# Performance work log

Hardware: AMD Instinct MI355X
Metric: run time of the kernel (lower is better)

The kernel has to match this reference:

```python
import jax, jax.numpy as jnp
import numpy as np

N_HEADS = 16

def kernel_sigmoid(x):
    return jax.nn.sigmoid(0.6053 * x - 4.102)

def setup_inputs() -> dict:
    key = jax.random.key(0)
    kq, kk, kv = jax.random.split(key, 3)
    B, LQ, LK, E = 4, 4096, 4096, 1024
    return {
        "Q": jax.random.normal(kq, (B, LQ, E), dtype=jnp.float32),
        "K": jax.random.normal(kk, (B, LK, E), dtype=jnp.float32),
        "V": jax.random.normal(kv, (B, LK, E), dtype=jnp.float32),
    }

def reference(Q, K, V):
    B, LQ, E = Q.shape
    LK = K.shape[1]
    H = N_HEADS
    D = E // H
    # split heads -> [B, H, L, D]
    Qh = Q.reshape(B, LQ, H, D).transpose(0, 2, 1, 3)
    Kh = K.reshape(B, LK, H, D).transpose(0, 2, 1, 3)
    Vh = V.reshape(B, LK, H, D).transpose(0, 2, 1, 3)
    phi_Q = kernel_sigmoid(Qh)           # [B,H,LQ,D]
    phi_K = kernel_sigmoid(Kh)           # [B,H,LK,D]
    # KV state: phi_K^T @ V -> [B,H,D,D]
    kv = jnp.einsum("bhkd,bhke->bhde", phi_K, Vh)
    num = jnp.einsum("bhqd,bhde->bhqe", phi_Q, kv)      # [B,H,LQ,D]
    k_sum = phi_K.sum(axis=2)                            # [B,H,D]
    den = jnp.einsum("bhqd,bhd->bhq", phi_Q, k_sum)      # [B,H,LQ]
    out = num / den[..., None]
    # merge heads -> [B, LQ, E]
    return out.transpose(0, 2, 1, 3).reshape(B, LQ, E)
```

## Files before the change

kernel.cpp:

```cpp
#include <hip/hip_runtime.h>
#include <cstdint>
#include <cstddef>

#define B_ 4
#define L_ 4096
#define E_ 1024
#define H_ 16
#define D_ 64
#define BH_ 64
#define ST2_ 4160
#define NCH_ 16
#define RPC_ (L_/NCH_)
#define NT_ (RPC_/32)

typedef __attribute__((ext_vector_type(8))) short short8v;
typedef __attribute__((ext_vector_type(4))) float f32x4;

__device__ __forceinline__ float sigk(float x) {
    return __builtin_amdgcn_rcpf(1.0f + __expf(4.102f - 0.6053f * x));
}
__device__ __forceinline__ unsigned short bfh(float f) {
    union { float f; unsigned u; } v; v.f = f;
    const unsigned r = v.u + 0x7fffu + ((v.u >> 16) & 1u);
    return (unsigned short)(r >> 16);
}
__device__ __forceinline__ float bf2f(unsigned short s) {
    union { unsigned u; float f; } v; v.u = ((unsigned)s) << 16;
    return v.f;
}


__global__ void __launch_bounds__(256) kv_partial_kernel(
    const float* __restrict__ K, const float* __restrict__ V,
    float* __restrict__ partial)
{
    __shared__ short8v Bfrag[2 * 8 * 64];

    const int ch = blockIdx.x & (NCH_ - 1);
    const int bh = blockIdx.x / NCH_;
    const int b = bh >> 4, h = bh & 15;
    const int tid = threadIdx.x;
    const int w = tid >> 6, l = tid & 63;
    const int g = l >> 4, m = l & 15;
    const int k4 = g << 2;
    const int col = (w << 4) + m;

    const float* Kp = K + (size_t)(b * L_ + ch * RPC_) * E_ + h * D_ + col;
    const float* Vp = V + (size_t)(b * L_ + ch * RPC_) * E_ + h * D_ + col;

    f32x4 acc[4];
    #pragma unroll
    for (int t = 0; t < 4; ++t) acc[t] = (f32x4){0.f, 0.f, 0.f, 0.f};
    float ksacc = 0.f;

    float kr[2][8], vr[2][8];
    #pragma unroll
    for (int j = 0; j < 8; ++j) {
        const int ko = k4 + (j & 3) + ((j >> 2) << 4);
        kr[0][j] = Kp[(size_t)ko * E_];
        vr[0][j] = Vp[(size_t)ko * E_];
    }
    {
        short8v Bh, Bl;
        #pragma unroll
        for (int j = 0; j < 8; ++j) {
            const unsigned short hb = bfh(vr[0][j]);
            Bh[j] = (short)hb;
            Bl[j] = (short)bfh(vr[0][j] - bf2f(hb));
        }
        Bfrag[(w << 1) * 64 + l]       = Bh;
        Bfrag[((w << 1) + 1) * 64 + l] = Bl;
    }
    #pragma unroll
    for (int j = 0; j < 8; ++j) {
        const int ko = 32 + k4 + (j & 3) + ((j >> 2) << 4);
        kr[1][j] = Kp[(size_t)ko * E_];
        vr[1][j] = Vp[(size_t)ko * E_];
    }
    asm volatile("s_waitcnt lgkmcnt(0)" ::: "memory");
    __builtin_amdgcn_sched_barrier(0);
    __builtin_amdgcn_s_barrier();

    #pragma unroll 2
    for (int t = 0; t < NT_; ++t) {
        const int cur = t & 1, nxt = cur ^ 1;
        short8v Ah;
        #pragma unroll
        for (int j = 0; j < 8; ++j) {
            const unsigned short hb = bfh(sigk(kr[cur][j]));
            Ah[j] = (short)hb;
            ksacc += bf2f(hb);
        }
        if (t + 2 < NT_) {
            #pragma unroll
            for (int j = 0; j < 8; ++j) {
                const int ko = ((t + 2) << 5) + k4 + (j & 3) + ((j >> 2) << 4);
                kr[cur][j] = Kp[(size_t)ko * E_];
                vr[cur][j] = Vp[(size_t)ko * E_];
            }
        }
        __builtin_amdgcn_sched_barrier(0);
        {
            const int buf = cur << 9;
            #pragma unroll
            for (int tt = 0; tt < 4; ++tt) {
                const short8v Bh = Bfrag[buf + (tt << 1) * 64 + l];
                const short8v Bl = Bfrag[buf + ((tt << 1) + 1) * 64 + l];
                acc[tt] = __builtin_amdgcn_mfma_f32_16x16x32_bf16(Ah, Bh, acc[tt], 0, 0, 0);
                acc[tt] = __builtin_amdgcn_mfma_f32_16x16x32_bf16(Ah, Bl, acc[tt], 0, 0, 0);
            }
        }
        if (t + 1 < NT_) {
            const int nb = nxt << 9;
            short8v Bh, Bl;
            #pragma unroll
            for (int j = 0; j < 8; ++j) {
                const unsigned short hb = bfh(vr[nxt][j]);
                Bh[j] = (short)hb;
                Bl[j] = (short)bfh(vr[nxt][j] - bf2f(hb));
            }
            Bfrag[nb + (w << 1) * 64 + l]       = Bh;
            Bfrag[nb + ((w << 1) + 1) * 64 + l] = Bl;
        }
        asm volatile("s_waitcnt lgkmcnt(0)" ::: "memory");
        __builtin_amdgcn_sched_barrier(0);
        __builtin_amdgcn_s_barrier();
    }

    ksacc += __shfl_xor(ksacc, 16);
    ksacc += __shfl_xor(ksacc, 32);

    const size_t pbase = ((size_t)ch * BH_ + bh) * ST2_;
    #pragma unroll
    for (int tt = 0; tt < 4; ++tt)
        #pragma unroll
        for (int r = 0; r < 4; ++r)
            partial[pbase + (size_t)((w << 4) + k4 + r) * 64 + (tt << 4) + m]
                = acc[tt][r];
    if (g == 0) partial[pbase + 4096 + (w << 4) + m] = ksacc;
}

__global__ void __launch_bounds__(256) kv_reduce_kernel(
    const float* __restrict__ partial, unsigned* __restrict__ kv2H,
    unsigned* __restrict__ kv2L, float* __restrict__ ksumf)
{
    const int bh = blockIdx.x >> 2, part = blockIdx.x & 3;
    const int tid = threadIdx.x;
    const int e = tid & 63;
    #pragma unroll
    for (int it = 0; it < 2; ++it) {
        const int pr = (tid >> 6) + (it << 2);
        const int d0 = (part << 4) + (pr << 1);
        float s0 = 0.f, s1 = 0.f;
        #pragma unroll
        for (int c = 0; c < NCH_; ++c) {
            const size_t pb = ((size_t)c * BH_ + bh) * ST2_;
            s0 += partial[pb + (d0 << 6) + e];
            s1 += partial[pb + ((d0 + 1) << 6) + e];
        }
        const unsigned short h0 = bfh(s0), h1 = bfh(s1);
        const unsigned short l0 = bfh(s0 - bf2f(h0));
        const unsigned short l1 = bfh(s1 - bf2f(h1));
        const int kk = d0 & 31;
        const int gg = (kk & 15) >> 2;
        const int jq = ((kk & 3) >> 1) + ((kk >> 4) << 1);
        const int lane = (e & 15) + (gg << 4);
        const int sp = ((d0 >> 5) << 2) + (e >> 4);
        const size_t idx = (size_t)bh * 2048 + (((sp << 6) + lane) << 2) + jq;
        kv2H[idx] = (unsigned)h0 | ((unsigned)h1 << 16);
        kv2L[idx] = (unsigned)l0 | ((unsigned)l1 << 16);
    }
    if (part == 0 && tid < 64) {
        float s = 0.f;
        #pragma unroll
        for (int c = 0; c < NCH_; ++c)
            s += partial[((size_t)c * BH_ + bh) * ST2_ + 4096 + tid];
        ksumf[bh * 64 + tid] = s;
    }
}

__global__ void __launch_bounds__(256) attn_out_kernel(
    const float* __restrict__ Q, const unsigned* __restrict__ kv2H,
    const unsigned* __restrict__ kv2L, const float* __restrict__ ksumf,
    float* __restrict__ out)
{
    __shared__ short8v kvH[8 * 64];
    __shared__ short8v kvL[8 * 64];
    __shared__ float Qt[64 * 65];

    const int bh = blockIdx.x >> 6, qb = blockIdx.x & 63;
    const int b = bh >> 4, h = bh & 15;
    const int tid = threadIdx.x;
    const int w = tid >> 6, l = tid & 63;
    const int g = l >> 4, m = l & 15;
    const int k4 = g << 2;
    const int rowb0 = qb << 6;

    {
        const uint4* srcH = (const uint4*)(kv2H + (size_t)bh * 2048);
        const uint4* srcL = (const uint4*)(kv2L + (size_t)bh * 2048);
        uint4* dH = (uint4*)kvH;
        uint4* dL = (uint4*)kvL;
        dH[tid]       = srcH[tid];
        dH[tid + 256] = srcH[tid + 256];
        dL[tid]       = srcL[tid];
        dL[tid + 256] = srcL[tid + 256];
    }
    #pragma unroll
    for (int i = 0; i < 4; ++i) {
        const int idx = tid + (i << 8);
        const int r = idx >> 4, c4i = (idx & 15) << 2;
        const float4 qv = *(const float4*)(
            Q + (size_t)(b * L_ + rowb0 + r) * E_ + h * D_ + c4i);
        float* qd = Qt + r * 65 + c4i;
        qd[0] = qv.x; qd[1] = qv.y; qd[2] = qv.z; qd[3] = qv.w;
    }
    float ksl[16];
    #pragma unroll
    for (int ji = 0; ji < 16; ++ji) {
        const int ks = ji >> 3, j = ji & 7;
        ksl[ji] = ksumf[bh * 64 + (ks << 5) + k4 + (j & 3) + ((j >> 2) << 4)];
    }
    __syncthreads();

    const int rl = (w << 4) + m;
    short8v Ah[2], Al[2];
    float den = 0.f;
    #pragma unroll
    for (int ks = 0; ks < 2; ++ks)
        #pragma unroll
        for (int j = 0; j < 8; ++j) {
            const float qv =
                Qt[rl * 65 + (ks << 5) + k4 + (j & 3) + ((j >> 2) << 4)];
            const float ph = sigk(qv);
            const unsigned short hb = bfh(ph);
            const unsigned short lb = bfh(ph - bf2f(hb));
            Ah[ks][j] = (short)hb;
            Al[ks][j] = (short)lb;
            den = fmaf(bf2f(hb) + bf2f(lb), ksl[(ks << 3) + j], den);
        }

    f32x4 acc[4];
    #pragma unroll
    for (int tt = 0; tt < 4; ++tt) acc[tt] = (f32x4){0.f, 0.f, 0.f, 0.f};
    #pragma unroll
    for (int ks = 0; ks < 2; ++ks)
        #pragma unroll
        for (int tt = 0; tt < 4; ++tt) {
            const int slot = (ks << 2) + tt;
            const short8v Bh = kvH[slot * 64 + l];
            const short8v Bl = kvL[slot * 64 + l];
            acc[tt] = __builtin_amdgcn_mfma_f32_16x16x32_bf16(Ah[ks], Bh, acc[tt], 0, 0, 0);
            acc[tt] = __builtin_amdgcn_mfma_f32_16x16x32_bf16(Ah[ks], Bl, acc[tt], 0, 0, 0);
            acc[tt] = __builtin_amdgcn_mfma_f32_16x16x32_bf16(Al[ks], Bh, acc[tt], 0, 0, 0);
        }

    den += __shfl_xor(den, 16);
    den += __shfl_xor(den, 32);
    float inv[4];
    #pragma unroll
    for (int r = 0; r < 4; ++r)
        inv[r] = __builtin_amdgcn_rcpf(__shfl(den, k4 + r));

    float* op = out + (size_t)(b * L_ + rowb0 + (w << 4)) * E_ + h * D_;
    #pragma unroll
    for (int tt = 0; tt < 4; ++tt)
        #pragma unroll
        for (int r = 0; r < 4; ++r)
            op[(size_t)(k4 + r) * E_ + (tt << 4) + m] = acc[tt][r] * inv[r];
}

extern "C" void kernel_launch(void* const* d_in, const int* in_sizes, int n_in,
                              void* d_out, int out_size, void* d_ws, size_t ws_size,
                              hipStream_t stream) {
    const float* Q = (const float*)d_in[0];
    const float* K = (const float*)d_in[1];
    const float* V = (const float*)d_in[2];
    float* out = (float*)d_out;

    float* partial = (float*)d_ws;
    unsigned* kv2H = (unsigned*)(partial + (size_t)NCH_ * BH_ * ST2_);
    unsigned* kv2L = kv2H + (size_t)BH_ * 2048;
    float* ksumf   = (float*)(kv2L + (size_t)BH_ * 2048);

    hipLaunchKernelGGL(kv_partial_kernel, dim3(BH_ * NCH_), dim3(256), 0, stream,
                       K, V, partial);
    hipLaunchKernelGGL(kv_reduce_kernel, dim3(BH_ * 4), dim3(256), 0, stream,
                       partial, kv2H, kv2L, ksumf);
    hipLaunchKernelGGL(attn_out_kernel, dim3(BH_ * 64), dim3(256), 0, stream,
                       Q, kv2H, kv2L, ksumf, out);
}
```

Measured before the change: 67.80 us.

## Stage raw K/V tiles in LDS via float4 coalesced loads in kv_partial

Replaces the per-thread strided scalar global loads of K and V, which sent each wave's values straight into MFMA fragment registers, with float4 row loads staged as raw fp32 tiles in padded shared memory. Each wave then reads its fragments from LDS and does the sigmoid and bf16 hi/lo split there. The aim is fewer, wider global memory transactions. In exchange, V is converted four times (once per wave) instead of once, and LDS traffic rises with scalar strided reads.

```diff
diff --git a/kernel.cpp b/kernel.cpp
--- a/kernel.cpp
+++ b/kernel.cpp
@@ -12,6 +12,7 @@
 #define NCH_ 16
 #define RPC_ (L_/NCH_)
 #define NT_ (RPC_/32)
+#define LDK_ 68
 
 typedef __attribute__((ext_vector_type(8))) short short8v;
 typedef __attribute__((ext_vector_type(4))) float f32x4;
@@ -34,7 +35,7 @@
     const float* __restrict__ K, const float* __restrict__ V,
     float* __restrict__ partial)
 {
-    __shared__ short8v Bfrag[2 * 8 * 64];
+    __shared__ float raw[2][2][32 * LDK_];
 
     const int ch = blockIdx.x & (NCH_ - 1);
     const int bh = blockIdx.x / NCH_;
@@ -43,39 +44,32 @@
     const int w = tid >> 6, l = tid & 63;
     const int g = l >> 4, m = l & 15;
     const int k4 = g << 2;
-    const int col = (w << 4) + m;
-
-    const float* Kp = K + (size_t)(b * L_ + ch * RPC_) * E_ + h * D_ + col;
-    const float* Vp = V + (size_t)(b * L_ + ch * RPC_) * E_ + h * D_ + col;
+    const int colA = (w << 4) + m;
+    const int r0 = tid >> 4;
+    const int c4 = (tid & 15) << 2;
+
+    const float* Kg = K + (size_t)(b * L_ + ch * RPC_) * E_ + h * D_;
+    const float* Vg = V + (size_t)(b * L_ + ch * RPC_) * E_ + h * D_;
 
     f32x4 acc[4];
     #pragma unroll
     for (int t = 0; t < 4; ++t) acc[t] = (f32x4){0.f, 0.f, 0.f, 0.f};
     float ksacc = 0.f;
 
-    float kr[2][8], vr[2][8];
-    #pragma unroll
-    for (int j = 0; j < 8; ++j) {
-        const int ko = k4 + (j & 3) + ((j >> 2) << 4);
-        kr[0][j] = Kp[(size_t)ko * E_];
-        vr[0][j] = Vp[(size_t)ko * E_];
-    }
-    {
-        short8v Bh, Bl;
-        #pragma unroll
-        for (int j = 0; j < 8; ++j) {
-            const unsigned short hb = bfh(vr[0][j]);
-            Bh[j] = (short)hb;
-            Bl[j] = (short)bfh(vr[0][j] - bf2f(hb));
-        }
-        Bfrag[(w << 1) * 64 + l]       = Bh;
-        Bfrag[((w << 1) + 1) * 64 + l] = Bl;
-    }
-    #pragma unroll
-    for (int j = 0; j < 8; ++j) {
-        const int ko = 32 + k4 + (j & 3) + ((j >> 2) << 4);
-        kr[1][j] = Kp[(size_t)ko * E_];
-        vr[1][j] = Vp[(size_t)ko * E_];
+    float4 kreg[2][2], vreg[2][2];
+    #pragma unroll
+    for (int s = 0; s < 2; ++s)
+        #pragma unroll
+        for (int rr = 0; rr < 2; ++rr) {
+            const size_t go = (size_t)((s << 5) + r0 + (rr << 4)) * E_ + c4;
+            kreg[s][rr] = *(const float4*)(Kg + go);
+            vreg[s][rr] = *(const float4*)(Vg + go);
+        }
+    #pragma unroll
+    for (int rr = 0; rr < 2; ++rr) {
+        const int ro = (r0 + (rr << 4)) * LDK_ + c4;
+        *(float4*)&raw[0][0][ro] = kreg[0][rr];
+        *(float4*)&raw[0][1][ro] = vreg[0][rr];
     }
     asm volatile("s_waitcnt lgkmcnt(0)" ::: "memory");
     __builtin_amdgcn_sched_barrier(0);
@@ -84,43 +78,48 @@
     #pragma unroll 2
     for (int t = 0; t < NT_; ++t) {
         const int cur = t & 1, nxt = cur ^ 1;
-        short8v Ah;
-        #pragma unroll
-        for (int j = 0; j < 8; ++j) {
-            const unsigned short hb = bfh(sigk(kr[cur][j]));
-            Ah[j] = (short)hb;
-            ksacc += bf2f(hb);
+        if (t + 1 < NT_) {
+            #pragma unroll
+            for (int rr = 0; rr < 2; ++rr) {
+                const int ro = (r0 + (rr << 4)) * LDK_ + c4;
+                *(float4*)&raw[nxt][0][ro] = kreg[nxt][rr];
+                *(float4*)&raw[nxt][1][ro] = vreg[nxt][rr];
+            }
         }
         if (t + 2 < NT_) {
             #pragma unroll
-            for (int j = 0; j < 8; ++j) {
-                const int ko = ((t + 2) << 5) + k4 + (j & 3) + ((j >> 2) << 4);
-                kr[cur][j] = Kp[(size_t)ko * E_];
-                vr[cur][j] = Vp[(size_t)ko * E_];
+            for (int rr = 0; rr < 2; ++rr) {
+                const size_t go =
+                    (size_t)(((t + 2) << 5) + r0 + (rr << 4)) * E_ + c4;
+                kreg[cur][rr] = *(const float4*)(Kg + go);
+                vreg[cur][rr] = *(const float4*)(Vg + go);
             }
         }
         __builtin_amdgcn_sched_barrier(0);
         {
-            const int buf = cur << 9;
+            short8v Ah;
+            #pragma unroll
+            for (int j = 0; j < 8; ++j) {
+                const int k = k4 + (j & 3) + ((j >> 2) << 4);
+                const float kvv = raw[cur][0][k * LDK_ + colA];
+                const unsigned short hb = bfh(sigk(kvv));
+                Ah[j] = (short)hb;
+                ksacc += bf2f(hb);
+            }
             #pragma unroll
             for (int tt = 0; tt < 4; ++tt) {
-                const short8v Bh = Bfrag[buf + (tt << 1) * 64 + l];
-                const short8v Bl = Bfrag[buf + ((tt << 1) + 1) * 64 + l];
+                short8v Bh, Bl;
+                #pragma unroll
+                for (int j = 0; j < 8; ++j) {
+                    const int k = k4 + (j & 3) + ((j >> 2) << 4);
+                    const float vv = raw[cur][1][k * LDK_ + (tt << 4) + m];
+                    const unsigned short hv = bfh(vv);
+                    Bh[j] = (short)hv;
+                    Bl[j] = (short)bfh(vv - bf2f(hv));
+                }
                 acc[tt] = __builtin_amdgcn_mfma_f32_16x16x32_bf16(Ah, Bh, acc[tt], 0, 0, 0);
                 acc[tt] = __builtin_amdgcn_mfma_f32_16x16x32_bf16(Ah, Bl, acc[tt], 0, 0, 0);
             }
-        }
-        if (t + 1 < NT_) {
-            const int nb = nxt << 9;
-            short8v Bh, Bl;
-            #pragma unroll
-            for (int j = 0; j < 8; ++j) {
-                const unsigned short hb = bfh(vr[nxt][j]);
-                Bh[j] = (short)hb;
-                Bl[j] = (short)bfh(vr[nxt][j] - bf2f(hb));
-            }
-            Bfrag[nb + (w << 1) * 64 + l]       = Bh;
-            Bfrag[nb + ((w << 1) + 1) * 64 + l] = Bl;
         }
         asm volatile("s_waitcnt lgkmcnt(0)" ::: "memory");
         __builtin_amdgcn_sched_barrier(0);
```

Result: slower. 107.6 us (+58.8%).

## Split KV partial kernel across 8 waves, halving MFMA work per wave

Applied to the files above, without the earlier changes.

The KV-partial kernel now runs 512 threads per block. Eight waves split the output columns (e) into two halves, and only the first four waves load V and stage the bf16 hi/lo fragments into shared memory. Each wave does half the MFMAs and keeps half the accumulators, which raises parallelism and latency hiding in the first stage. The cost is that K is loaded and passed through the sigmoid twice (both e-halves recompute phi_K), plus extra barrier participants.

```diff
diff --git a/kernel.cpp b/kernel.cpp
--- a/kernel.cpp
+++ b/kernel.cpp
@@ -30,7 +30,7 @@
 }
 
 
-__global__ void __launch_bounds__(256) kv_partial_kernel(
+__global__ void __launch_bounds__(512) kv_partial_kernel(
     const float* __restrict__ K, const float* __restrict__ V,
     float* __restrict__ partial)
 {
@@ -41,16 +41,20 @@
     const int b = bh >> 4, h = bh & 15;
     const int tid = threadIdx.x;
     const int w = tid >> 6, l = tid & 63;
+    const int ds = w & 3, eh = w >> 2;
     const int g = l >> 4, m = l & 15;
     const int k4 = g << 2;
-    const int col = (w << 4) + m;
-
-    const float* Kp = K + (size_t)(b * L_ + ch * RPC_) * E_ + h * D_ + col;
-    const float* Vp = V + (size_t)(b * L_ + ch * RPC_) * E_ + h * D_ + col;
-
-    f32x4 acc[4];
-    #pragma unroll
-    for (int t = 0; t < 4; ++t) acc[t] = (f32x4){0.f, 0.f, 0.f, 0.f};
+    const int colK = (ds << 4) + m;
+    const int colV = (w << 4) + m;
+    const bool stager = (w < 4);
+    const bool doks = (eh == 0);
+
+    const float* Kp = K + (size_t)(b * L_ + ch * RPC_) * E_ + h * D_ + colK;
+    const float* Vp = V + (size_t)(b * L_ + ch * RPC_) * E_ + h * D_ + colV;
+
+    f32x4 acc[2];
+    acc[0] = (f32x4){0.f, 0.f, 0.f, 0.f};
+    acc[1] = (f32x4){0.f, 0.f, 0.f, 0.f};
     float ksacc = 0.f;
 
     float kr[2][8], vr[2][8];
@@ -58,9 +62,9 @@
     for (int j = 0; j < 8; ++j) {
         const int ko = k4 + (j & 3) + ((j >> 2) << 4);
         kr[0][j] = Kp[(size_t)ko * E_];
-        vr[0][j] = Vp[(size_t)ko * E_];
-    }
-    {
+        if (stager) vr[0][j] = Vp[(size_t)ko * E_];
+    }
+    if (stager) {
         short8v Bh, Bl;
         #pragma unroll
         for (int j = 0; j < 8; ++j) {
@@ -75,7 +79,7 @@
     for (int j = 0; j < 8; ++j) {
         const int ko = 32 + k4 + (j & 3) + ((j >> 2) << 4);
         kr[1][j] = Kp[(size_t)ko * E_];
-        vr[1][j] = Vp[(size_t)ko * E_];
+        if (stager) vr[1][j] = Vp[(size_t)ko * E_];
     }
     asm volatile("s_waitcnt lgkmcnt(0)" ::: "memory");
     __builtin_amdgcn_sched_barrier(0);
@@ -89,28 +93,29 @@
         for (int j = 0; j < 8; ++j) {
             const unsigned short hb = bfh(sigk(kr[cur][j]));
             Ah[j] = (short)hb;
-            ksacc += bf2f(hb);
+            if (doks) ksacc += bf2f(hb);
         }
         if (t + 2 < NT_) {
             #pragma unroll
             for (int j = 0; j < 8; ++j) {
                 const int ko = ((t + 2) << 5) + k4 + (j & 3) + ((j >> 2) << 4);
                 kr[cur][j] = Kp[(size_t)ko * E_];
-                vr[cur][j] = Vp[(size_t)ko * E_];
+                if (stager) vr[cur][j] = Vp[(size_t)ko * E_];
             }
         }
         __builtin_amdgcn_sched_barrier(0);
         {
             const int buf = cur << 9;
             #pragma unroll
-            for (int tt = 0; tt < 4; ++tt) {
+            for (int q = 0; q < 2; ++q) {
+                const int tt = (eh << 1) + q;
                 const short8v Bh = Bfrag[buf + (tt << 1) * 64 + l];
                 const short8v Bl = Bfrag[buf + ((tt << 1) + 1) * 64 + l];
-                acc[tt] = __builtin_amdgcn_mfma_f32_16x16x32_bf16(Ah, Bh, acc[tt], 0, 0, 0);
-                acc[tt] = __builtin_amdgcn_mfma_f32_16x16x32_bf16(Ah, Bl, acc[tt], 0, 0, 0);
+                acc[q] = __builtin_amdgcn_mfma_f32_16x16x32_bf16(Ah, Bh, acc[q], 0, 0, 0);
+                acc[q] = __builtin_amdgcn_mfma_f32_16x16x32_bf16(Ah, Bl, acc[q], 0, 0, 0);
             }
         }
-        if (t + 1 < NT_) {
+        if (stager && t + 1 < NT_) {
             const int nb = nxt << 9;
             short8v Bh, Bl;
             #pragma unroll
@@ -127,17 +132,21 @@
         __builtin_amdgcn_s_barrier();
     }
 
-    ksacc += __shfl_xor(ksacc, 16);
-    ksacc += __shfl_xor(ksacc, 32);
+    if (doks) {
+        ksacc += __shfl_xor(ksacc, 16);
+        ksacc += __shfl_xor(ksacc, 32);
+    }
 
     const size_t pbase = ((size_t)ch * BH_ + bh) * ST2_;
     #pragma unroll
-    for (int tt = 0; tt < 4; ++tt)
+    for (int q = 0; q < 2; ++q) {
+        const int tt = (eh << 1) + q;
         #pragma unroll
         for (int r = 0; r < 4; ++r)
-            partial[pbase + (size_t)((w << 4) + k4 + r) * 64 + (tt << 4) + m]
-                = acc[tt][r];
-    if (g == 0) partial[pbase + 4096 + (w << 4) + m] = ksacc;
+            partial[pbase + (size_t)((ds << 4) + k4 + r) * 64 + (tt << 4) + m]
+                = acc[q][r];
+    }
+    if (doks && g == 0) partial[pbase + 4096 + (ds << 4) + m] = ksacc;
 }
 
 __global__ void __launch_bounds__(256) kv_reduce_kernel(
@@ -283,7 +292,7 @@
     unsigned* kv2L = kv2H + (size_t)BH_ * 2048;
     float* ksumf   = (float*)(kv2L + (size_t)BH_ * 2048);
 
-    hipLaunchKernelGGL(kv_partial_kernel, dim3(BH_ * NCH_), dim3(256), 0, stream,
+    hipLaunchKernelGGL(kv_partial_kernel, dim3(BH_ * NCH_), dim3(512), 0, stream,
                        K, V, partial);
     hipLaunchKernelGGL(kv_reduce_kernel, dim3(BH_ * 4), dim3(256), 0, stream,
                        partial, kv2H, kv2L, ksumf);
```

After: 74.97 us. +10.6%, slower.

## Fuse KV reduction into partial kernel via last-block atomic counter; halve attn blocks

Applied to the files above, without the earlier changes.

Removes the separate kv_reduce kernel launch. The last chunk-block to finish for each (batch, head) now does the cross-chunk reduction and the bf16 hi/lo packing, detected through an atomic counter that a memset clears on every launch. The output kernel also handles two 64-row Q tiles per block, so the KV fragments staged in shared memory are reused and the block count is halved. The cost is a serialized tail where a single block reduces each head, plus an extra memset, and fewer blocks in flight for the output stage.

```diff
diff --git a/kernel.cpp b/kernel.cpp
--- a/kernel.cpp
+++ b/kernel.cpp
@@ -32,9 +32,12 @@
 
 __global__ void __launch_bounds__(256) kv_partial_kernel(
     const float* __restrict__ K, const float* __restrict__ V,
-    float* __restrict__ partial)
+    float* __restrict__ partial, unsigned* __restrict__ kv2H,
+    unsigned* __restrict__ kv2L, float* __restrict__ ksumf,
+    unsigned* __restrict__ cnt)
 {
     __shared__ short8v Bfrag[2 * 8 * 64];
+    __shared__ int lastflag;
 
     const int ch = blockIdx.x & (NCH_ - 1);
     const int bh = blockIdx.x / NCH_;
@@ -138,44 +141,49 @@
             partial[pbase + (size_t)((w << 4) + k4 + r) * 64 + (tt << 4) + m]
                 = acc[tt][r];
     if (g == 0) partial[pbase + 4096 + (w << 4) + m] = ksacc;
-}
-
-__global__ void __launch_bounds__(256) kv_reduce_kernel(
-    const float* __restrict__ partial, unsigned* __restrict__ kv2H,
-    unsigned* __restrict__ kv2L, float* __restrict__ ksumf)
-{
-    const int bh = blockIdx.x >> 2, part = blockIdx.x & 3;
-    const int tid = threadIdx.x;
-    const int e = tid & 63;
-    #pragma unroll
-    for (int it = 0; it < 2; ++it) {
-        const int pr = (tid >> 6) + (it << 2);
-        const int d0 = (part << 4) + (pr << 1);
-        float s0 = 0.f, s1 = 0.f;
-        #pragma unroll
-        for (int c = 0; c < NCH_; ++c) {
-            const size_t pb = ((size_t)c * BH_ + bh) * ST2_;
-            s0 += partial[pb + (d0 << 6) + e];
-            s1 += partial[pb + ((d0 + 1) << 6) + e];
-        }
-        const unsigned short h0 = bfh(s0), h1 = bfh(s1);
-        const unsigned short l0 = bfh(s0 - bf2f(h0));
-        const unsigned short l1 = bfh(s1 - bf2f(h1));
-        const int kk = d0 & 31;
-        const int gg = (kk & 15) >> 2;
-        const int jq = ((kk & 3) >> 1) + ((kk >> 4) << 1);
-        const int lane = (e & 15) + (gg << 4);
-        const int sp = ((d0 >> 5) << 2) + (e >> 4);
-        const size_t idx = (size_t)bh * 2048 + (((sp << 6) + lane) << 2) + jq;
-        kv2H[idx] = (unsigned)h0 | ((unsigned)h1 << 16);
-        kv2L[idx] = (unsigned)l0 | ((unsigned)l1 << 16);
-    }
-    if (part == 0 && tid < 64) {
-        float s = 0.f;
-        #pragma unroll
-        for (int c = 0; c < NCH_; ++c)
-            s += partial[((size_t)c * BH_ + bh) * ST2_ + 4096 + tid];
-        ksumf[bh * 64 + tid] = s;
+
+    __threadfence();
+    __syncthreads();
+    if (tid == 0)
+        lastflag = (atomicAdd(&cnt[bh], 1u) == (unsigned)(NCH_ - 1));
+    __syncthreads();
+    if (lastflag) {
+        __threadfence();
+        const int e = tid & 63;
+        #pragma unroll
+        for (int part = 0; part < 4; ++part) {
+            #pragma unroll
+            for (int it = 0; it < 2; ++it) {
+                const int pr = (tid >> 6) + (it << 2);
+                const int d0 = (part << 4) + (pr << 1);
+                float s0 = 0.f, s1 = 0.f;
+                #pragma unroll
+                for (int c = 0; c < NCH_; ++c) {
+                    const size_t pb = ((size_t)c * BH_ + bh) * ST2_;
+                    s0 += partial[pb + (d0 << 6) + e];
+                    s1 += partial[pb + ((d0 + 1) << 6) + e];
+                }
+                const unsigned short h0 = bfh(s0), h1 = bfh(s1);
+                const unsigned short l0 = bfh(s0 - bf2f(h0));
+                const unsigned short l1 = bfh(s1 - bf2f(h1));
+                const int kk = d0 & 31;
+                const int gg = (kk & 15) >> 2;
+                const int jq = ((kk & 3) >> 1) + ((kk >> 4) << 1);
+                const int lane = (e & 15) + (gg << 4);
+                const int sp = ((d0 >> 5) << 2) + (e >> 4);
+                const size_t idx =
+                    (size_t)bh * 2048 + (((sp << 6) + lane) << 2) + jq;
+                kv2H[idx] = (unsigned)h0 | ((unsigned)h1 << 16);
+                kv2L[idx] = (unsigned)l0 | ((unsigned)l1 << 16);
+            }
+        }
+        if (tid < 64) {
+            float s = 0.f;
+            #pragma unroll
+            for (int c = 0; c < NCH_; ++c)
+                s += partial[((size_t)c * BH_ + bh) * ST2_ + 4096 + tid];
+            ksumf[bh * 64 + tid] = s;
+        }
     }
 }
 
@@ -188,13 +196,12 @@
     __shared__ short8v kvL[8 * 64];
     __shared__ float Qt[64 * 65];
 
-    const int bh = blockIdx.x >> 6, qb = blockIdx.x & 63;
+    const int bh = blockIdx.x >> 5, qb = blockIdx.x & 31;
     const int b = bh >> 4, h = bh & 15;
     const int tid = threadIdx.x;
     const int w = tid >> 6, l = tid & 63;
     const int g = l >> 4, m = l & 15;
     const int k4 = g << 2;
-    const int rowb0 = qb << 6;
 
     {
         const uint4* srcH = (const uint4*)(kv2H + (size_t)bh * 2048);
@@ -206,68 +213,73 @@
         dL[tid]       = srcL[tid];
         dL[tid + 256] = srcL[tid + 256];
     }
-    #pragma unroll
-    for (int i = 0; i < 4; ++i) {
-        const int idx = tid + (i << 8);
-        const int r = idx >> 4, c4i = (idx & 15) << 2;
-        const float4 qv = *(const float4*)(
-            Q + (size_t)(b * L_ + rowb0 + r) * E_ + h * D_ + c4i);
-        float* qd = Qt + r * 65 + c4i;
-        qd[0] = qv.x; qd[1] = qv.y; qd[2] = qv.z; qd[3] = qv.w;
-    }
     float ksl[16];
     #pragma unroll
     for (int ji = 0; ji < 16; ++ji) {
         const int ks = ji >> 3, j = ji & 7;
         ksl[ji] = ksumf[bh * 64 + (ks << 5) + k4 + (j & 3) + ((j >> 2) << 4)];
     }
-    __syncthreads();
-
-    const int rl = (w << 4) + m;
-    short8v Ah[2], Al[2];
-    float den = 0.f;
-    #pragma unroll
-    for (int ks = 0; ks < 2; ++ks)
-        #pragma unroll
-        for (int j = 0; j < 8; ++j) {
-            const float qv =
-                Qt[rl * 65 + (ks << 5) + k4 + (j & 3) + ((j >> 2) << 4)];
-            const float ph = sigk(qv);
-            const unsigned short hb = bfh(ph);
-            const unsigned short lb = bfh(ph - bf2f(hb));
-            Ah[ks][j] = (short)hb;
-            Al[ks][j] = (short)lb;
-            den = fmaf(bf2f(hb) + bf2f(lb), ksl[(ks << 3) + j], den);
-        }
-
-    f32x4 acc[4];
-    #pragma unroll
-    for (int tt = 0; tt < 4; ++tt) acc[tt] = (f32x4){0.f, 0.f, 0.f, 0.f};
-    #pragma unroll
-    for (int ks = 0; ks < 2; ++ks)
-        #pragma unroll
-        for (int tt = 0; tt < 4; ++tt) {
-            const int slot = (ks << 2) + tt;
-            const short8v Bh = kvH[slot * 64 + l];
-            const short8v Bl = kvL[slot * 64 + l];
-            acc[tt] = __builtin_amdgcn_mfma_f32_16x16x32_bf16(Ah[ks], Bh, acc[tt], 0, 0, 0);
-            acc[tt] = __builtin_amdgcn_mfma_f32_16x16x32_bf16(Ah[ks], Bl, acc[tt], 0, 0, 0);
-            acc[tt] = __builtin_amdgcn_mfma_f32_16x16x32_bf16(Al[ks], Bh, acc[tt], 0, 0, 0);
-        }
-
-    den += __shfl_xor(den, 16);
-    den += __shfl_xor(den, 32);
-    float inv[4];
-    #pragma unroll
-    for (int r = 0; r < 4; ++r)
-        inv[r] = __builtin_amdgcn_rcpf(__shfl(den, k4 + r));
-
-    float* op = out + (size_t)(b * L_ + rowb0 + (w << 4)) * E_ + h * D_;
-    #pragma unroll
-    for (int tt = 0; tt < 4; ++tt)
+
+    for (int qt = 0; qt < 2; ++qt) {
+        const int rowb0 = ((qb << 1) + qt) << 6;
+        #pragma unroll
+        for (int i = 0; i < 4; ++i) {
+            const int idx = tid + (i << 8);
+            const int r = idx >> 4, c4i = (idx & 15) << 2;
+            const float4 qv = *(const float4*)(
+                Q + (size_t)(b * L_ + rowb0 + r) * E_ + h * D_ + c4i);
+            float* qd = Qt + r * 65 + c4i;
+            qd[0] = qv.x; qd[1] = qv.y; qd[2] = qv.z; qd[3] = qv.w;
+        }
+        __syncthreads();
+
+        const int rl = (w << 4) + m;
+        short8v Ah[2], Al[2];
+        float den = 0.f;
+        #pragma unroll
+        for (int ks = 0; ks < 2; ++ks)
+            #pragma unroll
+            for (int j = 0; j < 8; ++j) {
+                const float qv =
+                    Qt[rl * 65 + (ks << 5) + k4 + (j & 3) + ((j >> 2) << 4)];
+                const float ph = sigk(qv);
+                const unsigned short hb = bfh(ph);
+                const unsigned short lb = bfh(ph - bf2f(hb));
+                Ah[ks][j] = (short)hb;
+                Al[ks][j] = (short)lb;
+                den = fmaf(bf2f(hb) + bf2f(lb), ksl[(ks << 3) + j], den);
+            }
+
+        f32x4 acc[4];
+        #pragma unroll
+        for (int tt = 0; tt < 4; ++tt) acc[tt] = (f32x4){0.f, 0.f, 0.f, 0.f};
+        #pragma unroll
+        for (int ks = 0; ks < 2; ++ks)
+            #pragma unroll
+            for (int tt = 0; tt < 4; ++tt) {
+                const int slot = (ks << 2) + tt;
+                const short8v Bh = kvH[slot * 64 + l];
+                const short8v Bl = kvL[slot * 64 + l];
+                acc[tt] = __builtin_amdgcn_mfma_f32_16x16x32_bf16(Ah[ks], Bh, acc[tt], 0, 0, 0);
+                acc[tt] = __builtin_amdgcn_mfma_f32_16x16x32_bf16(Ah[ks], Bl, acc[tt], 0, 0, 0);
+                acc[tt] = __builtin_amdgcn_mfma_f32_16x16x32_bf16(Al[ks], Bh, acc[tt], 0, 0, 0);
+            }
+
+        den += __shfl_xor(den, 16);
+        den += __shfl_xor(den, 32);
+        float inv[4];
         #pragma unroll
         for (int r = 0; r < 4; ++r)
-            op[(size_t)(k4 + r) * E_ + (tt << 4) + m] = acc[tt][r] * inv[r];
+            inv[r] = __builtin_amdgcn_rcpf(__shfl(den, k4 + r));
+
+        float* op = out + (size_t)(b * L_ + rowb0 + (w << 4)) * E_ + h * D_;
+        #pragma unroll
+        for (int tt = 0; tt < 4; ++tt)
+            #pragma unroll
+            for (int r = 0; r < 4; ++r)
+                op[(size_t)(k4 + r) * E_ + (tt << 4) + m] = acc[tt][r] * inv[r];
+        __syncthreads();
+    }
 }
 
 extern "C" void kernel_launch(void* const* d_in, const int* in_sizes, int n_in,
@@ -282,11 +294,12 @@
     unsigned* kv2H = (unsigned*)(partial + (size_t)NCH_ * BH_ * ST2_);
     unsigned* kv2L = kv2H + (size_t)BH_ * 2048;
     float* ksumf   = (float*)(kv2L + (size_t)BH_ * 2048);
+    unsigned* cnt  = (unsigned*)(ksumf + BH_ * 64);
+
+    hipMemsetAsync(cnt, 0, BH_ * sizeof(unsigned), stream);
 
     hipLaunchKernelGGL(kv_partial_kernel, dim3(BH_ * NCH_), dim3(256), 0, stream,
-                       K, V, partial);
-    hipLaunchKernelGGL(kv_reduce_kernel, dim3(BH_ * 4), dim3(256), 0, stream,
-                       partial, kv2H, kv2L, ksumf);
-    hipLaunchKernelGGL(attn_out_kernel, dim3(BH_ * 64), dim3(256), 0, stream,
+                       K, V, partial, kv2H, kv2L, ksumf, cnt);
+    hipLaunchKernelGGL(attn_out_kernel, dim3(BH_ * 32), dim3(256), 0, stream,
                        Q, kv2H, kv2L, ksumf, out);
 }
```

Result: slower. 261.7 us (+286.1%).
